# Performance work log

Hardware: AMD Instinct MI355X
Metric: run time of the kernel (lower is better)

Reference implementation:

```python
import jax, jax.numpy as jnp
import numpy as np

B, C, H, W = 64, 512, 8, 8
K = 100            # num_class
H1, HID, L = 64, 128, 32   # ae_hidden[0], fixed hidd, ae_latent
CLIP = 100.0       # CSSRClassifier.clip_len
RED = -0.1         # model='pcssr' -> -1, times gamma=0.1
PUSH_THRESH = 10000.0


def setup_inputs() -> dict:
    key = jax.random.key(0)
    ks = jax.random.split(key, 9)
    s = lambda fan_in: 1.0 / np.sqrt(fan_in)  # kaiming-ish 1x1 conv init scale
    return {
        "x": jax.random.normal(ks[0], (B, C, H, W), jnp.float32),
        "ycls": jax.random.randint(ks[1], (B,), 0, K),
        "safe_margin_all": jax.random.normal(ks[2], (K,), jnp.float32),
        "safe_distance_all": jax.random.normal(ks[3], (K,), jnp.float32),
        "W1": jax.random.normal(ks[4], (K, H1, C), jnp.float32) * s(C),
        "W2": jax.random.normal(ks[5], (K, HID, H1), jnp.float32) * s(H1),
        "W3": jax.random.normal(ks[6], (K, L, HID), jnp.float32) * s(HID),
        "prototypes": jax.random.normal(ks[7], (K, L, H, W), jnp.float32),
        "prototypes1": jax.random.normal(ks[8], (K, L, H, W), jnp.float32),
    }


def reference(x, ycls, safe_margin_all, safe_distance_all, W1, W2, W3, prototypes, prototypes1):
    P = H * W
    xf = x.reshape(B, C, P)
    # per-class 1x1-conv encoder (tanh after every conv), batched over classes k
    h = jnp.tanh(jnp.einsum('koc,bcp->kbop', W1, xf))      # [K,B,H1,P]
    h = jnp.tanh(jnp.einsum('koi,kbip->kbop', W2, h))      # [K,B,HID,P]
    lt = jnp.tanh(jnp.einsum('koi,kbip->kbop', W3, h))     # [K,B,L,P]
    p = prototypes.reshape(K, 1, L, P)
    p1 = prototypes1.reshape(K, 1, L, P)
    # squared-L2 distance over channel dim, scaled by reduction, clipped
    er = jnp.clip(jnp.sum((lt - p) ** 2, axis=2) * RED, -CLIP, CLIP)    # [K,B,P]
    er1 = jnp.clip(jnp.sum((lt - p1) ** 2, axis=2) * RED, -CLIP, CLIP)  # [K,B,P]
    # training losses (pull on er1, push on er), vectorized across classes
    f = jnp.sum(er, axis=2)    # [K,B] spatial-summed errors
    f1 = jnp.sum(er1, axis=2)  # [K,B]
    cls_ids = jnp.arange(K)[:, None]
    mask_eq = (ycls[None, :] == cls_ids).astype(f.dtype)   # [K,B]
    n_eq = jnp.sum(mask_eq, axis=1)
    pull = jnp.sum(jnp.where(n_eq > 0,
                             jnp.sum(f1 * mask_eq, axis=1) / jnp.maximum(n_eq, 1.0),
                             0.0))
    comb = (1.0 - mask_eq) * (f < PUSH_THRESH).astype(f.dtype)
    n_comb = jnp.sum(comb, axis=1)
    push = jnp.sum(jnp.where(n_comb > 0,
                             jnp.sum(f * comb, axis=1) / jnp.maximum(n_comb, 1.0),
                             0.0))
    # cat per-class [B,1,H,W] errors along dim 1 -> [B,K,H,W]
    logits = jnp.transpose(er, (1, 0, 2)).reshape(B, K, H, W)
    logits1 = jnp.transpose(er1, (1, 0, 2)).reshape(B, K, H, W)
    return logits, logits1, pull, push
```

## Files before the change

### kernel.cpp

```cpp
#include <hip/hip_runtime.h>

typedef short  s16x8  __attribute__((ext_vector_type(8)));
typedef float  f32x16 __attribute__((ext_vector_type(16)));
typedef unsigned short u16;
typedef unsigned long long u64b;

#define MFMA32(a,b,c) __builtin_amdgcn_mfma_f32_32x32x16_bf16((a),(b),(c),0,0,0)
#define KCLS 100

__device__ __forceinline__ u16 f2bf(float f) {
  return (u16)(__builtin_bit_cast(unsigned, f) >> 16);
}

__device__ __forceinline__ unsigned pk2(float lo, float hi) {
  return __builtin_amdgcn_perm(__builtin_bit_cast(unsigned, hi),
                               __builtin_bit_cast(unsigned, lo), 0x07060302u);
}
__device__ __forceinline__ u64b pk4(float v0, float v1, float v2, float v3) {
  return (u64b)pk2(v0, v1) | ((u64b)pk2(v2, v3) << 32);
}

__device__ __forceinline__ float tanh_poly(float x) {
  float xc = fminf(fmaxf(x, -2.5f), 2.5f);
  float t = xc * xc;
  float g = fmaf(fmaf(fmaf(t, -0.0029255f, 0.043897f), t, -0.255307f), t, 0.985857f);
  return xc * g;
}

__device__ __forceinline__ void ld_lds16(const void* g, void* l) {
  __builtin_amdgcn_global_load_lds(
      (const __attribute__((address_space(1))) unsigned char*)g,
      (__attribute__((address_space(3))) unsigned char*)l, 16, 0, 0);
}

__global__ void prep(const float* __restrict__ x, const float* __restrict__ w1,
                     const float* __restrict__ w2, const float* __restrict__ w3,
                     u16* __restrict__ xF, u16* __restrict__ W1F,
                     u16* __restrict__ W2F, u16* __restrict__ W3F,
                     float* __restrict__ fz, float* __restrict__ out2) {
  __shared__ float tile[64][65];
  const int bid = blockIdx.x, t = threadIdx.x;
  if (bid == 0 && t < 2) out2[t] = 0.f;
  if (bid < 512) {
    const int b = bid >> 3, ck = bid & 7;
    #pragma unroll
    for (int j = 0; j < 4; j++) {
      int e4 = j * 1024 + t * 4;
      int c = e4 >> 6, p0 = e4 & 63;
      float4 v = *(const float4*)(x + ((size_t)b * 512 + ck * 64 + c) * 64 + p0);
      tile[c][p0] = v.x; tile[c][p0 + 1] = v.y; tile[c][p0 + 2] = v.z; tile[c][p0 + 3] = v.w;
    }
    __syncthreads();
    #pragma unroll
    for (int i = 0; i < 2; i++) {
      int s = i * 256 + t;
      int ksl = s >> 7, ph = (s >> 6) & 1, lane = s & 63;
      int cb = ksl * 16 + (lane >> 5) * 8, pp = ph * 32 + (lane & 31);
      u16 o[8];
      #pragma unroll
      for (int jj = 0; jj < 8; jj++) o[jj] = f2bf(tile[cb + jj][pp]);
      *(uint4*)(xF + (((size_t)b * 64 + (ck * 4 + ksl) * 2 + ph) * 512) + lane * 8) = *(uint4*)o;
    }
  } else if (bid < 1312) {
    int base = (bid - 512) * 512;
    #pragma unroll
    for (int i = 0; i < 2; i++) {
      int s = base + i * 256 + t;
      int frag = s >> 6, lane = s & 63;
      int k = frag >> 6, fr = frag & 63;
      int m = (fr & 1) * 32 + (lane & 31);
      int c0 = (fr >> 1) * 16 + (lane >> 5) * 8;
      const float* src = w1 + ((size_t)k * 64 + m) * 512 + c0;
      float4 a = *(const float4*)src, b4 = *(const float4*)(src + 4);
      u16 o[8] = { f2bf(a.x), f2bf(a.y), f2bf(a.z), f2bf(a.w),
                   f2bf(b4.x), f2bf(b4.y), f2bf(b4.z), f2bf(b4.w) };
      *(uint4*)(W1F + ((size_t)frag * 512) + lane * 8) = *(uint4*)o;
    }
  } else if (bid < 1512) {
    int base = (bid - 1312) * 512;
    #pragma unroll
    for (int i = 0; i < 2; i++) {
      int s = base + i * 256 + t;
      int frag = s >> 6, lane = s & 63;
      int k = frag >> 4, fr = frag & 15;
      int m = (fr & 3) * 32 + (lane & 31);
      int c0 = (fr >> 2) * 16 + (lane >> 5) * 8;
      const float* src = w2 + ((size_t)k * 128 + m) * 64 + c0;
      float4 a = *(const float4*)src, b4 = *(const float4*)(src + 4);
      u16 o[8] = { f2bf(a.x), f2bf(a.y), f2bf(a.z), f2bf(a.w),
                   f2bf(b4.x), f2bf(b4.y), f2bf(b4.z), f2bf(b4.w) };
      *(uint4*)(W2F + ((size_t)frag * 512) + lane * 8) = *(uint4*)o;
    }
  } else if (bid < 1612) {
    int base = (bid - 1512) * 512;
    #pragma unroll
    for (int i = 0; i < 2; i++) {
      int s = base + i * 256 + t;
      int frag = s >> 6, lane = s & 63;
      int k = frag >> 3, kb = frag & 7;
      int m = lane & 31;
      int c0 = kb * 16 + (lane >> 5) * 8;
      const float* src = w3 + ((size_t)k * 32 + m) * 128 + c0;
      float4 a = *(const float4*)src, b4 = *(const float4*)(src + 4);
      u16 o[8] = { f2bf(a.x), f2bf(a.y), f2bf(a.z), f2bf(a.w),
                   f2bf(b4.x), f2bf(b4.y), f2bf(b4.z), f2bf(b4.w) };
      *(uint4*)(W3F + ((size_t)frag * 512) + lane * 8) = *(uint4*)o;
    }
  } else {
    int i4 = (bid - 1612) * 256 + t;
    if (i4 < 3200) {
      float4 z = {0.f, 0.f, 0.f, 0.f};
      *(float4*)(fz + (size_t)i4 * 4) = z;
    }
  }
}

__global__ __launch_bounds__(256, 4) void cssr_main(
    const u16* __restrict__ W1F, const u16* __restrict__ W2F, const u16* __restrict__ W3F,
    const u16* __restrict__ xF, const float* __restrict__ protos,
    const float* __restrict__ protos1, float* __restrict__ out,
    float* __restrict__ fw, float* __restrict__ f1w)
{
  __shared__ u16 pool[16384];

  const int bid = blockIdx.x;
  const int kp = bid >> 6, b = bid & 63;
  const int tid = threadIdx.x, w = tid >> 6, lane = tid & 63;
  const int nhalf = lane >> 5, nn = lane & 31;
  const int kk = w >> 1, mt = w & 1;
  const int k = kp * 2 + kk;

  const u16* xb = xF + ((size_t)b * 64) * 512;

  #pragma unroll
  for (int i = 0; i < 2; i++) {
    int f = 2 * w + i;
    (void)f;
  }
  #pragma unroll
  for (int i = 0; i < 4; i++) {
    int f = w * 4 + i;
    ld_lds16(xb + (size_t)f * 512 + lane * 8, &pool[f * 512]);
  }
  __syncthreads();

  f32x16 acc1[2] = {};
  for (int ci = 0; ci < 4; ci++) {
    const int pb = ci & 1;
    if (ci < 3) {
      #pragma unroll
      for (int i = 0; i < 4; i++) {
        int f = w * 4 + i;
        ld_lds16(xb + (size_t)((ci + 1) * 16 + f) * 512 + lane * 8,
                 &pool[(pb ^ 1) * 8192 + f * 512]);
      }
    }
    #pragma unroll
    for (int ksl = 0; ksl < 8; ksl++) {
      s16x8 A = *(const s16x8*)(W1F + (((size_t)k * 64 + (ci * 8 + ksl) * 2 + mt) * 512) + lane * 8);
      #pragma unroll
      for (int nt = 0; nt < 2; nt++) {
        s16x8 B = *(const s16x8*)&pool[pb * 8192 + (ksl * 2 + nt) * 512 + lane * 8];
        acc1[nt] = MFMA32(A, B, acc1[nt]);
      }
    }
    __syncthreads();
  }

  #pragma unroll
  for (int nt = 0; nt < 2; nt++) {
    #pragma unroll
    for (int g = 0; g < 4; g++) {
      u64b hv = pk4(tanh_poly(acc1[nt][g * 4 + 0]), tanh_poly(acc1[nt][g * 4 + 1]),
                    tanh_poly(acc1[nt][g * 4 + 2]), tanh_poly(acc1[nt][g * 4 + 3]));
      int kb = mt * 2 + (g >> 1);
      int tl = (g & 1) * 32 + nn;
      *(u64b*)&pool[kk * 4096 + (kb * 2 + nt) * 512 + tl * 8 + nhalf * 4] = hv;
    }
  }
  __syncthreads();

  f32x16 acc2[2][2] = {};
  #pragma unroll
  for (int kb = 0; kb < 4; kb++) {
    s16x8 A0 = *(const s16x8*)(W2F + (((size_t)k * 16 + kb * 4 + mt * 2 + 0) * 512) + lane * 8);
    s16x8 A1 = *(const s16x8*)(W2F + (((size_t)k * 16 + kb * 4 + mt * 2 + 1) * 512) + lane * 8);
    #pragma unroll
    for (int nh = 0; nh < 2; nh++) {
      s16x8 B = *(const s16x8*)&pool[kk * 4096 + (kb * 2 + nh) * 512 + lane * 8];
      acc2[0][nh] = MFMA32(A0, B, acc2[0][nh]);
      acc2[1][nh] = MFMA32(A1, B, acc2[1][nh]);
    }
  }
  __syncthreads();

  #pragma unroll
  for (int m4l = 0; m4l < 2; m4l++) {
    #pragma unroll
    for (int nh = 0; nh < 2; nh++) {
      #pragma unroll
      for (int g = 0; g < 4; g++) {
        u64b hv = pk4(tanh_poly(acc2[m4l][nh][g * 4 + 0]), tanh_poly(acc2[m4l][nh][g * 4 + 1]),
                      tanh_poly(acc2[m4l][nh][g * 4 + 2]), tanh_poly(acc2[m4l][nh][g * 4 + 3]));
        int kb2 = mt * 4 + m4l * 2 + (g >> 1);
        int tl  = (g & 1) * 32 + nn;
        *(u64b*)&pool[kk * 8192 + (kb2 * 2 + nh) * 512 + tl * 8 + nhalf * 4] = hv;
      }
    }
  }
  __syncthreads();

  f32x16 acc3 = {};
  #pragma unroll
  for (int kb = 0; kb < 8; kb++) {
    s16x8 A = *(const s16x8*)(W3F + (((size_t)k * 8 + kb) * 512) + lane * 8);
    s16x8 B = *(const s16x8*)&pool[kk * 8192 + (kb * 2 + mt) * 512 + lane * 8];
    acc3 = MFMA32(A, B, acc3);
  }

  const int p = mt * 32 + nn;
  const float* pr  = protos  + (size_t)k * 2048;
  const float* pr1 = protos1 + (size_t)k * 2048;
  float d2 = 0.f, d21 = 0.f;
  #pragma unroll
  for (int g = 0; g < 4; g++) {
    #pragma unroll
    for (int q = 0; q < 4; q++) {
      int m = q + 8 * g + 4 * nhalf;
      float lt = tanh_poly(acc3[g * 4 + q]);
      float d = lt - pr [m * 64 + p];  d2  += d * d;
      float e = lt - pr1[m * 64 + p];  d21 += e * e;
    }
  }
  d2 += __shfl_xor(d2, 32); d21 += __shfl_xor(d21, 32);
  float er  = fminf(fmaxf(d2  * -0.1f, -100.f), 100.f);
  float er1 = fminf(fmaxf(d21 * -0.1f, -100.f), 100.f);
  if (nhalf == 0) {
    out[(size_t)b * 6400 + k * 64 + p]          = er;
    out[409600 + (size_t)b * 6400 + k * 64 + p] = er1;
  }
  float s = er, s1 = er1;
  s += __shfl_xor(s, 1);  s1 += __shfl_xor(s1, 1);
  s += __shfl_xor(s, 2);  s1 += __shfl_xor(s1, 2);
  s += __shfl_xor(s, 4);  s1 += __shfl_xor(s1, 4);
  s += __shfl_xor(s, 8);  s1 += __shfl_xor(s1, 8);
  s += __shfl_xor(s, 16); s1 += __shfl_xor(s1, 16);
  if (lane == 0) {
    atomicAdd(&fw [k * 64 + b], s);
    atomicAdd(&f1w[k * 64 + b], s1);
  }
}

__global__ void finalize(const float* __restrict__ f, const float* __restrict__ f1,
                         const int* __restrict__ ycls, float* __restrict__ out2) {
  const int k = blockIdx.x, b = threadIdx.x;
  float fv = f[k * 64 + b], f1v = f1[k * 64 + b];
  bool eq = (ycls[b] == k);
  bool cb = (!eq) && (fv < 10000.f);
  float s1 = eq ? f1v : 0.f, ne = eq ? 1.f : 0.f;
  float s  = cb ? fv  : 0.f, nc = cb ? 1.f : 0.f;
  #pragma unroll
  for (int o = 1; o < 64; o <<= 1) {
    s1 += __shfl_xor(s1, o); ne += __shfl_xor(ne, o);
    s  += __shfl_xor(s,  o); nc += __shfl_xor(nc, o);
  }
  if (b == 0) {
    if (ne > 0.f) atomicAdd(&out2[0], s1 / ne);
    if (nc > 0.f) atomicAdd(&out2[1], s / nc);
  }
}

extern "C" void kernel_launch(void* const* d_in, const int* in_sizes, int n_in,
                              void* d_out, int out_size, void* d_ws, size_t ws_size,
                              hipStream_t stream) {
  const float* x     = (const float*)d_in[0];
  const int*   ycls  = (const int*)d_in[1];
  const float* W1    = (const float*)d_in[4];
  const float* W2    = (const float*)d_in[5];
  const float* W3    = (const float*)d_in[6];
  const float* prot  = (const float*)d_in[7];
  const float* prot1 = (const float*)d_in[8];
  float* out = (float*)d_out;

  char* ws = (char*)d_ws;
  u16*  xFb = (u16*)(ws);
  u16*  W1F = (u16*)(ws + 4194304);
  u16*  W2F = (u16*)(ws + 10747904);
  u16*  W3F = (u16*)(ws + 12386304);
  float* fw  = (float*)(ws + 13205504);
  float* f1w = (float*)(ws + 13231104);

  prep<<<1625, 256, 0, stream>>>(x, W1, W2, W3, xFb, W1F, W2F, W3F,
                                 fw, out + 819200);
  cssr_main<<<50 * 64, 256, 0, stream>>>(W1F, W2F, W3F, xFb, prot, prot1,
                                         out, fw, f1w);
  finalize<<<KCLS, 64, 0, stream>>>(fw, f1w, ycls, out + 819200);
}
```

Baseline: 147.4 us.

## Fuse finalize into main kernel via last-block counter; use exp2-based tanh

Removes the separate finalize launch by having each main-kernel block bump a global done counter. The last block to finish reads the per-class sums and computes the pull and push losses. The counter is reset in prep. It also replaces the clamped polynomial tanh with an exp2/rcp hardware-intrinsic formulation, which costs fewer VALU ops and is more accurate. The cost is an extra atomic and threadfence per block, plus a serial tail reduction done by one block.

```diff
diff --git a/kernel.cpp b/kernel.cpp
--- a/kernel.cpp
+++ b/kernel.cpp
@@ -20,11 +20,9 @@
   return (u64b)pk2(v0, v1) | ((u64b)pk2(v2, v3) << 32);
 }
 
-__device__ __forceinline__ float tanh_poly(float x) {
-  float xc = fminf(fmaxf(x, -2.5f), 2.5f);
-  float t = xc * xc;
-  float g = fmaf(fmaf(fmaf(t, -0.0029255f, 0.043897f), t, -0.255307f), t, 0.985857f);
-  return xc * g;
+__device__ __forceinline__ float tanh_fast(float x) {
+  float e = __builtin_amdgcn_exp2f(x * 2.8853900817779268f);
+  return 1.0f - 2.0f * __builtin_amdgcn_rcpf(e + 1.0f);
 }
 
 __device__ __forceinline__ void ld_lds16(const void* g, void* l) {
@@ -37,10 +35,14 @@
                      const float* __restrict__ w2, const float* __restrict__ w3,
                      u16* __restrict__ xF, u16* __restrict__ W1F,
                      u16* __restrict__ W2F, u16* __restrict__ W3F,
-                     float* __restrict__ fz, float* __restrict__ out2) {
+                     float* __restrict__ fz, unsigned* __restrict__ done,
+                     float* __restrict__ out2) {
   __shared__ float tile[64][65];
   const int bid = blockIdx.x, t = threadIdx.x;
-  if (bid == 0 && t < 2) out2[t] = 0.f;
+  if (bid == 0) {
+    if (t < 2) out2[t] = 0.f;
+    if (t == 2) *done = 0u;
+  }
   if (bid < 512) {
     const int b = bid >> 3, ck = bid & 7;
     #pragma unroll
@@ -118,10 +120,12 @@
 __global__ __launch_bounds__(256, 4) void cssr_main(
     const u16* __restrict__ W1F, const u16* __restrict__ W2F, const u16* __restrict__ W3F,
     const u16* __restrict__ xF, const float* __restrict__ protos,
-    const float* __restrict__ protos1, float* __restrict__ out,
-    float* __restrict__ fw, float* __restrict__ f1w)
+    const float* __restrict__ protos1, const int* __restrict__ ycls,
+    float* __restrict__ out, float* __restrict__ fw, float* __restrict__ f1w,
+    unsigned* __restrict__ done, float* __restrict__ out2)
 {
   __shared__ u16 pool[16384];
+  __shared__ int isLast;
 
   const int bid = blockIdx.x;
   const int kp = bid >> 6, b = bid & 63;
@@ -133,11 +137,6 @@
   const u16* xb = xF + ((size_t)b * 64) * 512;
 
   #pragma unroll
-  for (int i = 0; i < 2; i++) {
-    int f = 2 * w + i;
-    (void)f;
-  }
-  #pragma unroll
   for (int i = 0; i < 4; i++) {
     int f = w * 4 + i;
     ld_lds16(xb + (size_t)f * 512 + lane * 8, &pool[f * 512]);
@@ -171,8 +170,8 @@
   for (int nt = 0; nt < 2; nt++) {
     #pragma unroll
     for (int g = 0; g < 4; g++) {
-      u64b hv = pk4(tanh_poly(acc1[nt][g * 4 + 0]), tanh_poly(acc1[nt][g * 4 + 1]),
-                    tanh_poly(acc1[nt][g * 4 + 2]), tanh_poly(acc1[nt][g * 4 + 3]));
+      u64b hv = pk4(tanh_fast(acc1[nt][g * 4 + 0]), tanh_fast(acc1[nt][g * 4 + 1]),
+                    tanh_fast(acc1[nt][g * 4 + 2]), tanh_fast(acc1[nt][g * 4 + 3]));
       int kb = mt * 2 + (g >> 1);
       int tl = (g & 1) * 32 + nn;
       *(u64b*)&pool[kk * 4096 + (kb * 2 + nt) * 512 + tl * 8 + nhalf * 4] = hv;
@@ -200,8 +199,8 @@
     for (int nh = 0; nh < 2; nh++) {
       #pragma unroll
       for (int g = 0; g < 4; g++) {
-        u64b hv = pk4(tanh_poly(acc2[m4l][nh][g * 4 + 0]), tanh_poly(acc2[m4l][nh][g * 4 + 1]),
-                      tanh_poly(acc2[m4l][nh][g * 4 + 2]), tanh_poly(acc2[m4l][nh][g * 4 + 3]));
+        u64b hv = pk4(tanh_fast(acc2[m4l][nh][g * 4 + 0]), tanh_fast(acc2[m4l][nh][g * 4 + 1]),
+                      tanh_fast(acc2[m4l][nh][g * 4 + 2]), tanh_fast(acc2[m4l][nh][g * 4 + 3]));
         int kb2 = mt * 4 + m4l * 2 + (g >> 1);
         int tl  = (g & 1) * 32 + nn;
         *(u64b*)&pool[kk * 8192 + (kb2 * 2 + nh) * 512 + tl * 8 + nhalf * 4] = hv;
@@ -227,7 +226,7 @@
     #pragma unroll
     for (int q = 0; q < 4; q++) {
       int m = q + 8 * g + 4 * nhalf;
-      float lt = tanh_poly(acc3[g * 4 + q]);
+      float lt = tanh_fast(acc3[g * 4 + q]);
       float d = lt - pr [m * 64 + p];  d2  += d * d;
       float e = lt - pr1[m * 64 + p];  d21 += e * e;
     }
@@ -249,24 +248,35 @@
     atomicAdd(&fw [k * 64 + b], s);
     atomicAdd(&f1w[k * 64 + b], s1);
   }
-}
-
-__global__ void finalize(const float* __restrict__ f, const float* __restrict__ f1,
-                         const int* __restrict__ ycls, float* __restrict__ out2) {
-  const int k = blockIdx.x, b = threadIdx.x;
-  float fv = f[k * 64 + b], f1v = f1[k * 64 + b];
-  bool eq = (ycls[b] == k);
-  bool cb = (!eq) && (fv < 10000.f);
-  float s1 = eq ? f1v : 0.f, ne = eq ? 1.f : 0.f;
-  float s  = cb ? fv  : 0.f, nc = cb ? 1.f : 0.f;
-  #pragma unroll
-  for (int o = 1; o < 64; o <<= 1) {
-    s1 += __shfl_xor(s1, o); ne += __shfl_xor(ne, o);
-    s  += __shfl_xor(s,  o); nc += __shfl_xor(nc, o);
-  }
-  if (b == 0) {
-    if (ne > 0.f) atomicAdd(&out2[0], s1 / ne);
-    if (nc > 0.f) atomicAdd(&out2[1], s / nc);
+
+  __threadfence();
+  if (tid == 0) isLast = (atomicAdd(done, 1u) == (unsigned)(KCLS * 32 - 1));
+  __syncthreads();
+  if (isLast) {
+    __threadfence();
+    int yv = ycls[lane];
+    float pull = 0.f, push = 0.f;
+    for (int k2 = w; k2 < KCLS; k2 += 4) {
+      float fv  = __hip_atomic_load(&fw [k2 * 64 + lane], __ATOMIC_RELAXED, __HIP_MEMORY_SCOPE_AGENT);
+      float f1v = __hip_atomic_load(&f1w[k2 * 64 + lane], __ATOMIC_RELAXED, __HIP_MEMORY_SCOPE_AGENT);
+      bool eq = (yv == k2);
+      bool cb = (!eq) && (fv < 10000.f);
+      float s1v = eq ? f1v : 0.f, ne = eq ? 1.f : 0.f;
+      float sv  = cb ? fv  : 0.f, nc = cb ? 1.f : 0.f;
+      #pragma unroll
+      for (int o = 1; o < 64; o <<= 1) {
+        s1v += __shfl_xor(s1v, o); ne += __shfl_xor(ne, o);
+        sv  += __shfl_xor(sv,  o); nc += __shfl_xor(nc, o);
+      }
+      if (lane == 0) {
+        if (ne > 0.f) pull += s1v / ne;
+        if (nc > 0.f) push += sv / nc;
+      }
+    }
+    if (lane == 0) {
+      atomicAdd(&out2[0], pull);
+      atomicAdd(&out2[1], push);
+    }
   }
 }
 
@@ -289,10 +299,10 @@
   u16*  W3F = (u16*)(ws + 12386304);
   float* fw  = (float*)(ws + 13205504);
   float* f1w = (float*)(ws + 13231104);
+  unsigned* done = (unsigned*)(ws + 13256704);
 
   prep<<<1625, 256, 0, stream>>>(x, W1, W2, W3, xFb, W1F, W2F, W3F,
-                                 fw, out + 819200);
-  cssr_main<<<50 * 64, 256, 0, stream>>>(W1F, W2F, W3F, xFb, prot, prot1,
-                                         out, fw, f1w);
-  finalize<<<KCLS, 64, 0, stream>>>(fw, f1w, ycls, out + 819200);
-}
+                                 fw, done, out + 819200);
+  cssr_main<<<50 * 64, 256, 0, stream>>>(W1F, W2F, W3F, xFb, prot, prot1, ycls,
+                                         out, fw, f1w, done, out + 819200);
+}
```

New measurement: 409.1 us. 2.77x slower.
